# Kernel optimization log

Measured on AMD Instinct MI355X. Metric: run time of the kernel, lower is better.

The kernel has to match this reference:

```python
import jax, jax.numpy as jnp
import numpy as np

B, N, D, H, R = 4, 4096, 1024, 16, 64
HD = D // H  # head_dim = 64


def setup_inputs() -> dict:
    key = jax.random.key(0)
    ks = jax.random.split(key, 8)
    x = jax.random.normal(ks[0], (B, N, D), dtype=jnp.float32)
    # nn.Linear weights are (out, in); y = x @ W.T
    Wq = jax.random.normal(ks[1], (D, D), dtype=jnp.float32) * (1.0 / np.sqrt(D))
    Wk = jax.random.normal(ks[2], (D, D), dtype=jnp.float32) * (1.0 / np.sqrt(D))
    Wv = jax.random.normal(ks[3], (D, D), dtype=jnp.float32) * (1.0 / np.sqrt(D))
    Wo = jax.random.normal(ks[4], (D, D), dtype=jnp.float32) * (1.0 / np.sqrt(D))
    bo = jnp.zeros((D,), dtype=jnp.float32)
    E = jax.random.normal(ks[5], (N, R), dtype=jnp.float32) * 0.02
    Fm = jax.random.normal(ks[6], (N, R), dtype=jnp.float32) * 0.02
    return {"x": x, "Wq": Wq, "Wk": Wk, "Wv": Wv, "Wo": Wo, "bo": bo, "E": E, "Fm": Fm}


def reference(x, Wq, Wk, Wv, Wo, bo, E, Fm):
    b, n, d = x.shape
    scale = np.sqrt(HD).astype(np.float32)
    # projections: torch Linear => x @ W.T ; reshape to (B, H, N, HD)
    def proj(W):
        y = jnp.einsum('bnd,ed->bne', x, W)
        return y.reshape(b, n, H, HD).transpose(0, 2, 1, 3)
    Q = proj(Wq)  # (B,H,N,HD)
    K = proj(Wk)
    V = proj(Wv)
    # low-rank projections along sequence: (B,H,R,HD)
    K_low = jnp.einsum('nr,bhnd->bhrd', E[:n], K)
    V_low = jnp.einsum('nr,bhnd->bhrd', Fm[:n], V)
    scores = jnp.einsum('bhnd,bhrd->bhnr', Q, K_low) / scale  # (B,H,N,R)
    attn = jax.nn.softmax(scores, axis=-1)
    out = jnp.einsum('bhnr,bhrd->bhnd', attn, V_low)  # (B,H,N,HD)
    out = out.transpose(0, 2, 1, 3).reshape(b, n, d)
    return jnp.einsum('bnd,ed->bne', out, Wo) + bo
```

## Files before the change

### kernel.cpp

```cpp
#include <hip/hip_runtime.h>
#include <stdint.h>

typedef __bf16 bf16;
typedef __bf16 bf16x8 __attribute__((ext_vector_type(8)));
typedef __bf16 bf16x4 __attribute__((ext_vector_type(4)));
typedef float  f32x4  __attribute__((ext_vector_type(4)));

#define NB   4096
#define DB   1024
#define RV   64
#define MB   16384

__global__ void detect_dtype(const unsigned short* x, int* flag) {
  __shared__ int cnt;
  if (threadIdx.x == 0) cnt = 0;
  __syncthreads();
  int local = 0;
  for (int i = threadIdx.x; i < 8192; i += 256) {
    const int e = (x[i] >> 7) & 0xFF;
    if (e >= 0xC0) local++;
  }
  atomicAdd(&cnt, local);
  __syncthreads();
  if (threadIdx.x == 0) *flag = (cnt > 64) ? 1 : 0;
}

struct CvtArgs {
  const void* src[8];
  bf16* dst[8];
  int n[8];
  int off[9];
};
__global__ void to_bf16_multi(CvtArgs a, const int* __restrict__ flag) {
  const int blk = blockIdx.x;
  int seg = 0;
#pragma unroll
  for (int s = 1; s < 8; ++s) seg += (blk >= a.off[s]);
  const int i = (blk - a.off[seg]) * 2048 + threadIdx.x * 8;
  if (i >= a.n[seg]) return;
  bf16* dst = a.dst[seg];
  if (*flag) {
    const float* s = (const float*)a.src[seg] + i;
    f32x4 x0 = *(const f32x4*)s;
    f32x4 x1 = *(const f32x4*)(s + 4);
    bf16x8 v;
    v[0]=(bf16)x0[0]; v[1]=(bf16)x0[1]; v[2]=(bf16)x0[2]; v[3]=(bf16)x0[3];
    v[4]=(bf16)x1[0]; v[5]=(bf16)x1[1]; v[6]=(bf16)x1[2]; v[7]=(bf16)x1[3];
    *(bf16x8*)(dst + i) = v;
  } else {
    *(uint4*)(dst + i) = *(const uint4*)((const bf16*)a.src[seg] + i);
  }
}

__global__ __launch_bounds__(256) void ef_transpose(
    const void* __restrict__ E, const void* __restrict__ F,
    bf16* __restrict__ EFt, const int* __restrict__ flag) {
  const int m = blockIdx.x;
  const int z = m >> 6, r = m & 63;
  const void* src = z ? F : E;
  const int t = threadIdx.x;
  bf16* dst = EFt + (size_t)m * 4096;
  if (*flag) {
    const float* s = (const float*)src;
#pragma unroll
    for (int i = 0; i < 16; ++i) {
      const int n = i*256 + t;
      dst[n] = (bf16)s[(size_t)n*RV + r];
    }
  } else {
    const bf16* s = (const bf16*)src;
#pragma unroll
    for (int i = 0; i < 16; ++i) {
      const int n = i*256 + t;
      dst[n] = s[(size_t)n*RV + r];
    }
  }
}

typedef __attribute__((address_space(1))) const void g_as1_void;
typedef __attribute__((address_space(3))) void as3_void;
static __device__ __forceinline__ void gload16(const void* g, void* l) {
  __builtin_amdgcn_global_load_lds((g_as1_void*)g, (as3_void*)l, 16, 0, 0);
}

__global__ __launch_bounds__(256, 4) void lowrank_mfma(
    const bf16* __restrict__ EFt, const bf16* __restrict__ xb,
    bf16* __restrict__ xEb, bf16* __restrict__ xFb) {
  const int b = blockIdx.x, dt = blockIdx.y;
  __shared__ __align__(16) bf16 sEF0[128*64];
  __shared__ __align__(16) bf16 sEF1[128*64];
  __shared__ __align__(16) bf16 sXT[32*64];
  const int t = threadIdx.x, lane = t & 63, w = t >> 6;
  const int lr = lane & 15, quad = lane >> 4;
  const int wm = (w & 1) * 64, wd = (w >> 1) * 16;

  const bf16* gA[4];
  int abase[4];
#pragma unroll
  for (int i = 0; i < 4; ++i) {
    const int c = i*256 + t, row = c >> 3, ch = c & 7;
    gA[i] = EFt + (size_t)row*4096 + (ch ^ (row & 7))*8;
    abase[i] = (i*256 + (w << 6)) * 8;
  }
  const bf16* gx = xb + ((size_t)b*NB + lane)*DB + dt*32 + w*8;
  int xslot[8];
#pragma unroll
  for (int j = 0; j < 8; ++j) {
    const int d = w*8 + j;
    xslot[j] = (d*8 + ((lane >> 3) ^ (d & 7)))*8 + (lane & 7);
  }
  f32x4 acc[4] = {};

  uint4 rx = *(const uint4*)gx;
#pragma unroll
  for (int i = 0; i < 4; ++i) gload16(gA[i], sEF0 + abase[i]);
  asm volatile("s_waitcnt vmcnt(0)" ::: "memory");
  __syncthreads();

  for (int kt = 0; kt < 4096; kt += 64) {
    {
      const bf16* px = (const bf16*)&rx;
#pragma unroll
      for (int j = 0; j < 8; ++j) sXT[xslot[j]] = px[j];
    }
    bf16* nbuf = ((kt >> 6) & 1) ? sEF0 : sEF1;
    if (kt + 64 < 4096) {
#pragma unroll
      for (int i = 0; i < 4; ++i) gload16(gA[i] + kt + 64, nbuf + abase[i]);
      rx = *(const uint4*)(gx + (size_t)(kt + 64)*DB);
    }
    asm volatile("s_waitcnt lgkmcnt(0)" ::: "memory");
    __syncthreads();
    const bf16* cbuf = ((kt >> 6) & 1) ? sEF1 : sEF0;
#pragma unroll
    for (int ks = 0; ks < 2; ++ks) {
      const int kc = ks*4 + quad;
      const int dd = wd + lr;
      bf16x8 bv = *(const bf16x8*)(sXT + (dd*8 + (kc ^ (dd & 7)))*8);
#pragma unroll
      for (int mi = 0; mi < 4; ++mi) {
        const int m = wm + mi*16 + lr;
        bf16x8 af = *(const bf16x8*)(cbuf + (m*8 + (kc ^ (m & 7)))*8);
        acc[mi] = __builtin_amdgcn_mfma_f32_16x16x32_bf16(af, bv, acc[mi], 0, 0, 0);
      }
    }
    if (kt + 64 < 4096) asm volatile("s_waitcnt vmcnt(1)" ::: "memory");
    __syncthreads();
  }

  bf16* dstbase = (wm == 0) ? xEb : xFb;
#pragma unroll
  for (int mi = 0; mi < 4; ++mi) {
    const int rowl = (wm + mi*16 + quad*4) & 63;
#pragma unroll
    for (int rg = 0; rg < 4; ++rg)
      dstbase[((size_t)b*64 + rowl + rg)*DB + dt*32 + wd + lr] = (bf16)acc[mi][rg];
  }
}

struct GemmArgs {
  const bf16* A;
  const bf16* B;
  void* C;
  const bf16* bias;
  const int* oflag;
  int force_f32;
  int M, N, K;
  const bf16* A2;
  const bf16* B2;
  void* C2;
  int dual;
};

__global__ __launch_bounds__(512, 2) void gemm_nt(GemmArgs args) {
  const int K = args.K, N = args.N;
  const bf16* Aptr = args.A;
  const bf16* Bptr = args.B;
  void* Cptr = args.C;
  __shared__ __align__(16) char smem[131072];
  bf16* const sA[4] = {(bf16*)smem,           (bf16*)(smem + 32768),
                       (bf16*)(smem + 65536), (bf16*)(smem + 98304)};
  bf16* const sB[4] = {(bf16*)(smem + 16384), (bf16*)(smem + 49152),
                       (bf16*)(smem + 81920), (bf16*)(smem + 114688)};

  const int t = threadIdx.x;
  const int lane = t & 63;
  const int w = t >> 6;
  const int lr = lane & 15;
  const int quad = lane >> 4;
  const int wm = (w >> 2) * 128;
  const int wn = (w & 3) * 64;

  int bx = blockIdx.x, by = blockIdx.y;
  if (args.dual) {
    if (by == 1) { Aptr = args.A2; Bptr = args.B2; Cptr = args.C2; }
    by = 0;
  } else if (gridDim.y == 64) {
    const int l = by * 4 + bx;
    const int xcd = l & 7, s = l >> 3;
    by = xcd * 8 + (s >> 2);
    bx = s & 3;
  }
  const int m0 = by * 256;
  const int n0 = bx * 256;

  const bf16* gA[2];
  const bf16* gB[2];
  int lds_off[2];
#pragma unroll
  for (int i = 0; i < 2; ++i) {
    const int c = i*512 + t, row = c >> 2, ch = c & 3;
    const int sc = ch ^ ((row >> 1) & 3);
    gA[i] = Aptr + (size_t)(m0 + row)*K + sc*8;
    gB[i] = Bptr + (size_t)(n0 + row)*K + sc*8;
    lds_off[i] = c * 8;
  }
  auto stage = [&](bf16* dA, bf16* dB, int ko) {
#pragma unroll
    for (int i = 0; i < 2; ++i) gload16(gA[i] + ko, dA + lds_off[i]);
#pragma unroll
    for (int i = 0; i < 2; ++i) gload16(gB[i] + ko, dB + lds_off[i]);
  };

  f32x4 acc[8][4] = {};

#define GSUB(J, WS, DOSTAGE) do {                                            \
    asm volatile("s_waitcnt " WS ::: "memory");                              \
    __syncthreads();                                                         \
    bf16x8 af[8], bv[4];                                                     \
    _Pragma("unroll")                                                        \
    for (int mi = 0; mi < 8; ++mi) {                                         \
      const int m = wm + mi*16 + lr;                                         \
      af[mi] = *(const bf16x8*)(sA[J] + m*32 + ((quad ^ ((m>>1)&3))*8));     \
    }                                                                        \
    _Pragma("unroll")                                                        \
    for (int ni = 0; ni < 4; ++ni) {                                         \
      const int n = wn + ni*16 + lr;                                         \
      bv[ni] = *(const bf16x8*)(sB[J] + n*32 + ((quad ^ ((n>>1)&3))*8));     \
    }                                                                        \
    if (DOSTAGE) stage(sA[((J)+3)&3], sB[((J)+3)&3], kt + ((J)+3)*32);       \
    __builtin_amdgcn_s_setprio(1);                                           \
    _Pragma("unroll")                                                        \
    for (int mi = 0; mi < 8; ++mi)                                           \
      _Pragma("unroll")                                                      \
      for (int ni = 0; ni < 4; ++ni)                                         \
        acc[mi][ni] = __builtin_amdgcn_mfma_f32_16x16x32_bf16(               \
            af[mi], bv[ni], acc[mi][ni], 0, 0, 0);                           \
    __builtin_amdgcn_s_setprio(0);                                           \
  } while (0)

  stage(sA[0], sB[0], 0);
  stage(sA[1], sB[1], 32);
  stage(sA[2], sB[2], 64);

  int kt = 0;
  for (; kt + 128 < K; kt += 128) {
    GSUB(0, "vmcnt(8)", 1);
    GSUB(1, "vmcnt(8)", 1);
    GSUB(2, "vmcnt(8)", 1);
    GSUB(3, "vmcnt(8)", 1);
  }
  GSUB(0, "vmcnt(8)", 1);
  GSUB(1, "vmcnt(8)", 0);
  GSUB(2, "vmcnt(4)", 0);
  GSUB(3, "vmcnt(0)", 0);
#undef GSUB

  __syncthreads();

  const int f32out = args.force_f32 | (args.oflag ? *args.oflag : 0);
  float* sEw = (float*)(smem + w * 16384);
#pragma unroll
  for (int h = 0; h < 2; ++h) {
    if (h) asm volatile("s_waitcnt lgkmcnt(0)" ::: "memory");
#pragma unroll
    for (int mi = 0; mi < 4; ++mi) {
#pragma unroll
      for (int ni = 0; ni < 4; ++ni) {
        const int colg = n0 + wn + ni*16 + lr;
        const float bvv = args.bias ? (float)args.bias[colg] : 0.0f;
#pragma unroll
        for (int rg = 0; rg < 4; ++rg) {
          const int row = mi*16 + quad*4 + rg;
          sEw[row*64 + ((ni*16 + lr) ^ ((row & 15)*4))] = acc[h*4 + mi][ni][rg] + bvv;
        }
      }
    }
    asm volatile("s_waitcnt lgkmcnt(0)" ::: "memory");
#pragma unroll
    for (int i = 0; i < 8; ++i) {
      const int c = i*64 + lane;
      const int row = c >> 3, ch = c & 7;
      const int d0 = ch * 8;
      const int swz = (row & 15) * 4;
      f32x4 v0 = *(const f32x4*)(sEw + row*64 + (d0 ^ swz));
      f32x4 v1 = *(const f32x4*)(sEw + row*64 + ((d0 + 4) ^ swz));
      const size_t base = (size_t)(m0 + wm + h*64 + row)*N + n0 + wn + d0;
      if (f32out) {
        *(f32x4*)((float*)Cptr + base)     = v0;
        *(f32x4*)((float*)Cptr + base + 4) = v1;
      } else {
        bf16x8 wv;
        wv[0]=(bf16)v0[0]; wv[1]=(bf16)v0[1]; wv[2]=(bf16)v0[2]; wv[3]=(bf16)v0[3];
        wv[4]=(bf16)v1[0]; wv[5]=(bf16)v1[1]; wv[6]=(bf16)v1[2]; wv[7]=(bf16)v1[3];
        *(bf16x8*)((bf16*)Cptr + base) = wv;
      }
    }
  }
}

__global__ __launch_bounds__(256, 2) void attn_mfma(
    const bf16* Q, const float* __restrict__ Klow,
    const float* __restrict__ Vlow, bf16* AO) {
  const int bh = blockIdx.x, b = bh >> 4, h = bh & 15;
  const int n0 = blockIdx.y * 128;

  __shared__ bf16 sQ[128*64];
  __shared__ bf16 sKb[64*64];
  __shared__ bf16 sVt[64*64];
  __shared__ bf16 sP[4][32*64];

  const int t = threadIdx.x;
  const int lane = t & 63;
  const int w = t >> 6;
  const int lr = lane & 15;
  const int quad = lane >> 4;

#pragma unroll
  for (int i = 0; i < 4; ++i) {
    const int c = i*256 + t;
    const int row = c >> 3, j = c & 7;
    const uint4 v = *(const uint4*)(Q + ((size_t)b*NB + n0 + row)*DB + h*64 + j*8);
    *(uint4*)(sQ + (row*8 + (j ^ (row & 7)))*8) = v;
  }
  {
    const int r = t >> 2, c0 = (t & 3) * 16;
    const float* kb = Klow + (size_t)(b*64 + r)*DB + h*64 + c0;
    const float* vb = Vlow + (size_t)(b*64 + r)*DB + h*64 + c0;
    float kf[16], vf[16];
#pragma unroll
    for (int i = 0; i < 4; ++i) {
      *(f32x4*)(kf + i*4) = *(const f32x4*)(kb + i*4);
      *(f32x4*)(vf + i*4) = *(const f32x4*)(vb + i*4);
    }
#pragma unroll
    for (int cc = 0; cc < 2; ++cc) {
      bf16x8 pk;
#pragma unroll
      for (int j2 = 0; j2 < 8; ++j2) pk[j2] = (bf16)kf[cc*8 + j2];
      const int ch = (c0 >> 3) + cc;
      *(bf16x8*)(sKb + (r*8 + (ch ^ (r & 7)))*8) = pk;
    }
#pragma unroll
    for (int j2 = 0; j2 < 16; ++j2) {
      const int d = c0 + j2;
      sVt[d*64 + (((r >> 3) ^ (d & 7))*8) + (r & 7)] = (bf16)vf[j2];
    }
  }
  __syncthreads();

  f32x4 accS[2][4] = {};
#pragma unroll
  for (int ks = 0; ks < 2; ++ks) {
    const int kc = ks*4 + quad;
    bf16x8 af[2], bv[4];
#pragma unroll
    for (int mi = 0; mi < 2; ++mi) {
      const int m = w*32 + mi*16 + lr;
      af[mi] = *(const bf16x8*)(sQ + (m*8 + (kc ^ (m & 7)))*8);
    }
#pragma unroll
    for (int ni = 0; ni < 4; ++ni) {
      const int r = ni*16 + lr;
      bv[ni] = *(const bf16x8*)(sKb + (r*8 + (kc ^ (r & 7)))*8);
    }
#pragma unroll
    for (int mi = 0; mi < 2; ++mi)
#pragma unroll
      for (int ni = 0; ni < 4; ++ni)
        accS[mi][ni] = __builtin_amdgcn_mfma_f32_16x16x32_bf16(
            af[mi], bv[ni], accS[mi][ni], 0, 0, 0);
  }

  float inv_[2][4];
#pragma unroll
  for (int mi = 0; mi < 2; ++mi)
#pragma unroll
    for (int rg = 0; rg < 4; ++rg) {
      float mv = -3.0e38f;
#pragma unroll
      for (int ni = 0; ni < 4; ++ni) mv = fmaxf(mv, accS[mi][ni][rg]);
#pragma unroll
      for (int d = 1; d < 16; d <<= 1) mv = fmaxf(mv, __shfl_xor(mv, d));
      float sum = 0.0f;
#pragma unroll
      for (int ni = 0; ni < 4; ++ni) {
        const float p = __expf((accS[mi][ni][rg] - mv) * 0.125f);
        accS[mi][ni][rg] = p;
        sum += p;
      }
#pragma unroll
      for (int d = 1; d < 16; d <<= 1) sum += __shfl_xor(sum, d);
      inv_[mi][rg] = 1.0f / sum;
    }

  bf16* myP = sP[w];
#pragma unroll
  for (int mi = 0; mi < 2; ++mi)
#pragma unroll
    for (int ni = 0; ni < 4; ++ni)
#pragma unroll
      for (int rg = 0; rg < 4; ++rg) {
        const int row = mi*16 + quad*4 + rg;
        const int col = ni*16 + lr;
        myP[row*64 + ((col >> 3) ^ (row & 7))*8 + (col & 7)] = (bf16)accS[mi][ni][rg];
      }

  f32x4 accO[2][4] = {};
#pragma unroll
  for (int ks = 0; ks < 2; ++ks) {
    const int kc = ks*4 + quad;
    bf16x8 ap[2], bvv[4];
#pragma unroll
    for (int mi = 0; mi < 2; ++mi) {
      const int m = mi*16 + lr;
      ap[mi] = *(const bf16x8*)(myP + (m*8 + (kc ^ (m & 7)))*8);
    }
#pragma unroll
    for (int di = 0; di < 4; ++di) {
      const int d = di*16 + lr;
      bvv[di] = *(const bf16x8*)(sVt + (d*8 + (kc ^ (d & 7)))*8);
    }
#pragma unroll
    for (int mi = 0; mi < 2; ++mi)
#pragma unroll
      for (int di = 0; di < 4; ++di)
        accO[mi][di] = __builtin_amdgcn_mfma_f32_16x16x32_bf16(
            ap[mi], bvv[di], accO[mi][di], 0, 0, 0);
  }

#pragma unroll
  for (int mi = 0; mi < 2; ++mi)
#pragma unroll
    for (int di = 0; di < 4; ++di)
#pragma unroll
      for (int rg = 0; rg < 4; ++rg) {
        const int row = mi*16 + quad*4 + rg;
        const int col = di*16 + lr;
        myP[row*64 + ((col >> 3) ^ (row & 7))*8 + (col & 7)] =
            (bf16)(accO[mi][di][rg] * inv_[mi][rg]);
      }
  asm volatile("s_waitcnt lgkmcnt(0)" ::: "memory");
#pragma unroll
  for (int i = 0; i < 4; ++i) {
    const int c = i*64 + lane;
    const int row = c >> 3, ch = c & 7;
    const bf16x8 v = *(const bf16x8*)(myP + row*64 + ((ch ^ (row & 7))*8));
    *(bf16x8*)(AO + ((size_t)b*NB + n0 + w*32 + row)*DB + h*64 + ch*8) = v;
  }
}

extern "C" void kernel_launch(void* const* d_in, const int* in_sizes, int n_in,
                              void* d_out, int out_size, void* d_ws, size_t ws_size,
                              hipStream_t stream) {
  char* ws = (char*)d_ws;
  const size_t MiB = 1024*1024;
  int*   flag = (int*)ws;
  float* Klow = (float*)(ws + 1*MiB);
  float* Vlow = (float*)(ws + 2*MiB);
  bf16*  xEb  = (bf16*)(ws + 3*MiB);
  bf16*  xFb  = (bf16*)(ws + 3*MiB + 512*1024);
  bf16*  EFt  = (bf16*)(ws + 4*MiB);
  bf16*  Wqb  = (bf16*)(ws + 7*MiB);
  bf16*  Wkb  = (bf16*)(ws + 9*MiB);
  bf16*  Wvb  = (bf16*)(ws + 11*MiB);
  bf16*  Wob  = (bf16*)(ws + 13*MiB);
  bf16*  bob  = (bf16*)(ws + 15*MiB);
  bf16*  xb   = (bf16*)(ws + 20*MiB);
  bf16*  S0   = (bf16*)(ws + 52*MiB);

  detect_dtype<<<1, 256, 0, stream>>>((const unsigned short*)d_in[0], flag);

  ef_transpose<<<dim3(128), 256, 0, stream>>>(d_in[6], d_in[7], EFt, flag);

  CvtArgs ca;
  bf16* dsts[6] = {xb, Wqb, Wkb, Wvb, Wob, bob};
  int   ns[6]   = {16777216, 1048576, 1048576, 1048576, 1048576, 1024};
  int off = 0;
  for (int i = 0; i < 6; ++i) {
    ca.src[i] = d_in[i]; ca.dst[i] = dsts[i]; ca.n[i] = ns[i];
    ca.off[i] = off; off += (ns[i] + 2047) / 2048;
  }
  for (int i = 6; i < 8; ++i) {
    ca.src[i] = d_in[0]; ca.dst[i] = xb; ca.n[i] = 0; ca.off[i] = off;
  }
  ca.off[8] = off;
  to_bf16_multi<<<dim3(off), 256, 0, stream>>>(ca, flag);

  lowrank_mfma<<<dim3(4, 32), 256, 0, stream>>>(EFt, xb, xEb, xFb);

  GemmArgs ka;
  ka.A = xEb; ka.B = Wkb; ka.C = Klow;
  ka.A2 = xFb; ka.B2 = Wvb; ka.C2 = Vlow;
  ka.dual = 1;
  ka.bias = nullptr; ka.oflag = nullptr; ka.force_f32 = 1;
  ka.M = 256; ka.N = DB; ka.K = DB;
  gemm_nt<<<dim3(4, 2), 512, 0, stream>>>(ka);

  GemmArgs qa;
  qa.A = xb; qa.B = Wqb; qa.C = S0; qa.bias = nullptr;
  qa.oflag = nullptr; qa.force_f32 = 0;
  qa.A2 = nullptr; qa.B2 = nullptr; qa.C2 = nullptr; qa.dual = 0;
  qa.M = MB; qa.N = DB; qa.K = DB;
  gemm_nt<<<dim3(4, 64), 512, 0, stream>>>(qa);

  attn_mfma<<<dim3(64, 32), 256, 0, stream>>>(S0, Klow, Vlow, S0);

  GemmArgs oa;
  oa.A = S0; oa.B = Wob; oa.C = d_out; oa.bias = bob;
  oa.oflag = flag; oa.force_f32 = 0;
  oa.A2 = nullptr; oa.B2 = nullptr; oa.C2 = nullptr; oa.dual = 0;
  oa.M = MB; oa.N = DB; oa.K = DB;
  gemm_nt<<<dim3(4, 64), 512, 0, stream>>>(oa);
}
```

Baseline: 334.0 us.

## Split low-rank sequence reduction across segments with a separate reduce kernel

The low-rank projection kernel (E^T x, F^T x) previously launched only 128 blocks, each looping over the full 4096-long sequence. It now splits the sequence into 8 segments across a third grid dimension, writes fp32 partial sums to workspace, and adds a small reduction kernel that sums the partials and converts them to bf16. This raises parallelism to fill the GPU's compute units, at the cost of an extra launch and about 16 MiB of partial-sum traffic. The partial buffer reuses the S0 workspace region, which is only written later by the Q GEMM.

Result: faster. 304.1 us (-8.9%).

```diff
diff --git a/kernel.cpp b/kernel.cpp
--- a/kernel.cpp
+++ b/kernel.cpp
@@ -10,6 +10,7 @@
 #define DB   1024
 #define RV   64
 #define MB   16384
+#define NSEG 8
 
 __global__ void detect_dtype(const unsigned short* x, int* flag) {
   __shared__ int cnt;
@@ -85,24 +86,25 @@
 
 __global__ __launch_bounds__(256, 4) void lowrank_mfma(
     const bf16* __restrict__ EFt, const bf16* __restrict__ xb,
-    bf16* __restrict__ xEb, bf16* __restrict__ xFb) {
-  const int b = blockIdx.x, dt = blockIdx.y;
+    float* __restrict__ Pf) {
+  const int b = blockIdx.x, dt = blockIdx.y, seg = blockIdx.z;
   __shared__ __align__(16) bf16 sEF0[128*64];
   __shared__ __align__(16) bf16 sEF1[128*64];
   __shared__ __align__(16) bf16 sXT[32*64];
   const int t = threadIdx.x, lane = t & 63, w = t >> 6;
   const int lr = lane & 15, quad = lane >> 4;
   const int wm = (w & 1) * 64, wd = (w >> 1) * 16;
+  const int nbase = seg * (NB / NSEG);
 
   const bf16* gA[4];
   int abase[4];
 #pragma unroll
   for (int i = 0; i < 4; ++i) {
     const int c = i*256 + t, row = c >> 3, ch = c & 7;
-    gA[i] = EFt + (size_t)row*4096 + (ch ^ (row & 7))*8;
+    gA[i] = EFt + (size_t)row*4096 + nbase + (ch ^ (row & 7))*8;
     abase[i] = (i*256 + (w << 6)) * 8;
   }
-  const bf16* gx = xb + ((size_t)b*NB + lane)*DB + dt*32 + w*8;
+  const bf16* gx = xb + ((size_t)b*NB + nbase + lane)*DB + dt*32 + w*8;
   int xslot[8];
 #pragma unroll
   for (int j = 0; j < 8; ++j) {
@@ -117,14 +119,14 @@
   asm volatile("s_waitcnt vmcnt(0)" ::: "memory");
   __syncthreads();
 
-  for (int kt = 0; kt < 4096; kt += 64) {
+  for (int kt = 0; kt < NB/NSEG; kt += 64) {
     {
       const bf16* px = (const bf16*)&rx;
 #pragma unroll
       for (int j = 0; j < 8; ++j) sXT[xslot[j]] = px[j];
     }
     bf16* nbuf = ((kt >> 6) & 1) ? sEF0 : sEF1;
-    if (kt + 64 < 4096) {
+    if (kt + 64 < NB/NSEG) {
 #pragma unroll
       for (int i = 0; i < 4; ++i) gload16(gA[i] + kt + 64, nbuf + abase[i]);
       rx = *(const uint4*)(gx + (size_t)(kt + 64)*DB);
@@ -144,18 +146,37 @@
         acc[mi] = __builtin_amdgcn_mfma_f32_16x16x32_bf16(af, bv, acc[mi], 0, 0, 0);
       }
     }
-    if (kt + 64 < 4096) asm volatile("s_waitcnt vmcnt(1)" ::: "memory");
+    if (kt + 64 < NB/NSEG) asm volatile("s_waitcnt vmcnt(1)" ::: "memory");
     __syncthreads();
   }
 
-  bf16* dstbase = (wm == 0) ? xEb : xFb;
+  float* dst = Pf + (((size_t)seg*4 + b)*128)*DB + dt*32 + wd + lr;
 #pragma unroll
   for (int mi = 0; mi < 4; ++mi) {
-    const int rowl = (wm + mi*16 + quad*4) & 63;
+    const int row128 = wm + mi*16 + quad*4;
 #pragma unroll
     for (int rg = 0; rg < 4; ++rg)
-      dstbase[((size_t)b*64 + rowl + rg)*DB + dt*32 + wd + lr] = (bf16)acc[mi][rg];
-  }
+      dst[(size_t)(row128 + rg)*DB] = acc[mi][rg];
+  }
+}
+
+__global__ __launch_bounds__(256) void lowrank_reduce(
+    const float* __restrict__ Pf, bf16* __restrict__ xEb, bf16* __restrict__ xFb) {
+  const int idx = blockIdx.x*256 + threadIdx.x;
+  const int d4  = idx & 255;
+  const int row = (idx >> 8) & 127;
+  const int b   = idx >> 15;
+  const float* p = Pf + ((size_t)b*128 + row)*DB + d4*4;
+  f32x4 s = {};
+#pragma unroll
+  for (int seg = 0; seg < NSEG; ++seg) {
+    f32x4 v = *(const f32x4*)(p + (size_t)seg*4*128*DB);
+    s[0]+=v[0]; s[1]+=v[1]; s[2]+=v[2]; s[3]+=v[3];
+  }
+  bf16x4 o;
+  o[0]=(bf16)s[0]; o[1]=(bf16)s[1]; o[2]=(bf16)s[2]; o[3]=(bf16)s[3];
+  bf16* dst = (row < 64 ? xEb : xFb) + ((size_t)b*64 + (row & 63))*DB + d4*4;
+  *(bf16x4*)dst = o;
 }
 
 struct GemmArgs {
@@ -478,6 +499,7 @@
   bf16*  bob  = (bf16*)(ws + 15*MiB);
   bf16*  xb   = (bf16*)(ws + 20*MiB);
   bf16*  S0   = (bf16*)(ws + 52*MiB);
+  float* Pf   = (float*)(ws + 52*MiB);
 
   detect_dtype<<<1, 256, 0, stream>>>((const unsigned short*)d_in[0], flag);
 
@@ -497,7 +519,8 @@
   ca.off[8] = off;
   to_bf16_multi<<<dim3(off), 256, 0, stream>>>(ca, flag);
 
-  lowrank_mfma<<<dim3(4, 32), 256, 0, stream>>>(EFt, xb, xEb, xFb);
+  lowrank_mfma<<<dim3(4, 32, NSEG), 256, 0, stream>>>(EFt, xb, Pf);
+  lowrank_reduce<<<dim3(512), 256, 0, stream>>>(Pf, xEb, xFb);
 
   GemmArgs ka;
   ka.A = xEb; ka.B = Wkb; ka.C = Klow;
```
